# Performance work log

Hardware: AMD Instinct MI355X
Metric: run time of the kernel (lower is better)

## Reference

```python
import jax, jax.numpy as jnp
import numpy as np

DROPOUT_P = 0.1  # module-level constant in the source
DROP_KEY = jax.random.key(42)

B, H, S, D = 4, 16, 1024, 64


def setup_inputs() -> dict:
    key = jax.random.key(0)
    kq, kk, kv = jax.random.split(key, 3)
    return {
        "query": jax.random.normal(kq, (B, H, S, D), dtype=jnp.float32),
        "key": jax.random.normal(kk, (B, H, S, D), dtype=jnp.float32),
        "value": jax.random.normal(kv, (B, H, S, D), dtype=jnp.float32),
        "scale_factor": 8,
    }


def reference(query, key, value, scale_factor):
    # qk = query @ key^T                         [B,H,S,S]
    qk = jnp.einsum("bhqd,bhkd->bhqk", query, key)
    # source divides by inv_scale = 1/scale_factor -> multiply by scale_factor
    scaled_qk = qk * jnp.float32(scale_factor)
    softmax_qk = jax.nn.softmax(scaled_qk, axis=-1)
    # inverted dropout with fixed key (deterministic reference)
    keep = jax.random.bernoulli(DROP_KEY, 1.0 - DROPOUT_P, softmax_qk.shape)
    dropout_qk = jnp.where(keep, softmax_qk / (1.0 - DROPOUT_P), 0.0)
    # output = attn @ value                      [B,H,S,D]
    return jnp.einsum("bhqk,bhkd->bhqd", dropout_qk, value)
```

## Files before the change

### kernel.cpp

```cpp
#include <hip/hip_runtime.h>
#include <stdint.h>
#include <math.h>


constexpr int Bn = 4, Hn = 16, Sn = 1024, Dn = 64;
constexpr int NT = 256;
constexpr int TQ = 128, TK = 64;
constexpr int CAP = 256;

typedef short s16x8 __attribute__((ext_vector_type(8)));
typedef short s16x4 __attribute__((ext_vector_type(4)));
typedef float f32x4 __attribute__((ext_vector_type(4)));

__device__ __forceinline__ uint16_t f2bf(float x) {
  uint32_t u = __float_as_uint(x);
  return (uint16_t)((u + 0x7fffu + ((u >> 16) & 1u)) >> 16);
}
__device__ __forceinline__ float bf2f(uint16_t h) {
  return __uint_as_float(((uint32_t)h) << 16);
}

__device__ __forceinline__ void tf_round(uint32_t& x0, uint32_t& x1, const int r) {
  x0 += x1;
  x1 = (x1 << r) | (x1 >> (32 - r));
  x1 ^= x0;
}

__device__ __noinline__ int keep_bit(uint32_t j) {
  uint32_t x0 = 0u, x1 = j;
  const uint32_t k0 = 0u, k1v = 42u;
  const uint32_t k2v = k0 ^ k1v ^ 0x1BD11BDAu;
  x0 += k0; x1 += k1v;
  tf_round(x0, x1, 13); tf_round(x0, x1, 15); tf_round(x0, x1, 26); tf_round(x0, x1, 6);
  x0 += k1v; x1 += k2v + 1u;
  tf_round(x0, x1, 17); tf_round(x0, x1, 29); tf_round(x0, x1, 16); tf_round(x0, x1, 24);
  x0 += k2v; x1 += k0 + 2u;
  tf_round(x0, x1, 13); tf_round(x0, x1, 15); tf_round(x0, x1, 26); tf_round(x0, x1, 6);
  x0 += k0; x1 += k1v + 3u;
  tf_round(x0, x1, 17); tf_round(x0, x1, 29); tf_round(x0, x1, 16); tf_round(x0, x1, 24);
  x0 += k1v; x1 += k2v + 4u;
  tf_round(x0, x1, 13); tf_round(x0, x1, 15); tf_round(x0, x1, 26); tf_round(x0, x1, 6);
  x0 += k2v; x1 += k0 + 5u;
  uint32_t bits = x0 ^ x1;
  float u = __uint_as_float((bits >> 9) | 0x3f800000u) - 1.0f;
  return u < 0.9f;
}

__global__ __launch_bounds__(NT) void prep_kv(const float* __restrict__ K,
                                              const float* __restrict__ V,
                                              uint16_t* __restrict__ Khg,
                                              uint16_t* __restrict__ Klg,
                                              uint16_t* __restrict__ Vtg) {
  __shared__ float Vl[TK][Dn + 1];
  const int t = threadIdx.x;
  const int kt = blockIdx.x;
  const int bh = blockIdx.y;
  const int r = t >> 2, qd = t & 3;
  const size_t tile = ((size_t)bh * 16 + kt) * 4096;
  const float* ksrc = K + ((size_t)bh * Sn + (size_t)(kt * TK + r)) * Dn + qd * 16;
  const float* vsrc = V + ((size_t)bh * Sn + (size_t)(kt * TK + r)) * Dn + qd * 16;

#pragma unroll
  for (int half = 0; half < 2; ++half) {
    float4 a = *(const float4*)(ksrc + half * 8);
    float4 b = *(const float4*)(ksrc + half * 8 + 4);
    float xs[8] = {a.x, a.y, a.z, a.w, b.x, b.y, b.z, b.w};
    s16x8 hv, lv;
#pragma unroll
    for (int j = 0; j < 8; ++j) {
      uint16_t hb = f2bf(xs[j]);
      hv[j] = (short)hb;
      lv[j] = (short)f2bf(xs[j] - bf2f(hb));
    }
    const int sc = (qd * 2 + half) ^ (r & 7);
    *(s16x8*)&Khg[tile + (size_t)r * 64 + sc * 8] = hv;
    *(s16x8*)&Klg[tile + (size_t)r * 64 + sc * 8] = lv;
    float4 va = *(const float4*)(vsrc + half * 8);
    float4 vb = *(const float4*)(vsrc + half * 8 + 4);
    *(float4*)&Vl[r][qd * 16 + half * 8] = va;
    *(float4*)&Vl[r][qd * 16 + half * 8 + 4] = vb;
  }
  __syncthreads();
#pragma unroll
  for (int half = 0; half < 2; ++half) {
    s16x8 ov;
#pragma unroll
    for (int j = 0; j < 8; ++j) ov[j] = (short)f2bf(Vl[qd * 16 + half * 8 + j][r]);
    const int sc = (qd * 2 + half) ^ (r & 7);
    *(s16x8*)&Vtg[tile + (size_t)r * 64 + sc * 8] = ov;
  }
}

__global__ __launch_bounds__(NT, 2) void attn_mfma6(
    const float* __restrict__ Q, const uint16_t* __restrict__ Khg,
    const uint16_t* __restrict__ Klg, const uint16_t* __restrict__ Vtg,
    const float* __restrict__ V, const int* __restrict__ scale_ptr,
    float* __restrict__ out) {
  __shared__ uint16_t KhS[TK * Dn];
  __shared__ uint16_t KlS[TK * Dn];
  __shared__ uint16_t VtS[TK * Dn];
  __shared__ uint16_t PS[4 * 32 * 64];
  __shared__ uint32_t Lm[4][CAP];
  __shared__ float Lsv[4][CAP];
  __shared__ float mfin[4][32];

  const int t = threadIdx.x;
  const int w = t >> 6;
  const int lane = t & 63;
  const int l16 = lane & 15;
  const int quad = lane >> 4;
  const int xl = l16 & 7;

  const int b = blockIdx.z, h = blockIdx.y;
  const int qbase = blockIdx.x * TQ;
  const int bh = b * Hn + h;
  const float qscale = (float)(*scale_ptr);
  const float pthr = 1.670170079e-5f;

  const int e0off = (w * 2) * 512 + lane * 8;
  const int e1off = (w * 2 + 1) * 512 + lane * 8;
  const size_t tbase = (size_t)bh * 16 * 4096;
  const int psw = w * 2048;

  s16x8 qh[2][2], ql[2][2];
#pragma unroll
  for (int u = 0; u < 2; ++u) {
    const int qrow = qbase + w * 32 + u * 16 + l16;
    const float* src = Q + ((size_t)bh * Sn + (size_t)qrow) * Dn;
#pragma unroll
    for (int ks = 0; ks < 2; ++ks) {
      float4 x0 = *(const float4*)(src + ks * 32 + quad * 8);
      float4 x1 = *(const float4*)(src + ks * 32 + quad * 8 + 4);
      float xv[8] = {x0.x, x0.y, x0.z, x0.w, x1.x, x1.y, x1.z, x1.w};
#pragma unroll
      for (int j = 0; j < 8; ++j) {
        const float xs = xv[j] * qscale;
        uint16_t hb = f2bf(xs);
        qh[u][ks][j] = (short)hb;
        ql[u][ks][j] = (short)f2bf(xs - bf2f(hb));
      }
    }
  }

  float m_r[2] = {-INFINITY, -INFINITY};
  float l_r[2] = {0.0f, 0.0f};
  f32x4 o_acc[2][4];
#pragma unroll
  for (int u = 0; u < 2; ++u)
#pragma unroll
    for (int c = 0; c < 4; ++c) o_acc[u][c] = (f32x4){0.f, 0.f, 0.f, 0.f};

  const uint32_t hbase = (uint32_t)bh * (uint32_t)Sn;
  int lbase = 0;

  for (int kt = 0; kt < Sn / TK; ++kt) {
    const int kbase = kt * TK;
    __syncthreads();

    {
      const size_t tile = tbase + (size_t)kt * 4096;
      __builtin_amdgcn_global_load_lds(
          (const __attribute__((address_space(1))) uint32_t*)(Khg + tile + e0off),
          (__attribute__((address_space(3))) uint32_t*)(KhS + e0off), 16, 0, 0);
      __builtin_amdgcn_global_load_lds(
          (const __attribute__((address_space(1))) uint32_t*)(Khg + tile + e1off),
          (__attribute__((address_space(3))) uint32_t*)(KhS + e1off), 16, 0, 0);
      __builtin_amdgcn_global_load_lds(
          (const __attribute__((address_space(1))) uint32_t*)(Klg + tile + e0off),
          (__attribute__((address_space(3))) uint32_t*)(KlS + e0off), 16, 0, 0);
      __builtin_amdgcn_global_load_lds(
          (const __attribute__((address_space(1))) uint32_t*)(Klg + tile + e1off),
          (__attribute__((address_space(3))) uint32_t*)(KlS + e1off), 16, 0, 0);
      __builtin_amdgcn_global_load_lds(
          (const __attribute__((address_space(1))) uint32_t*)(Vtg + tile + e0off),
          (__attribute__((address_space(3))) uint32_t*)(VtS + e0off), 16, 0, 0);
      __builtin_amdgcn_global_load_lds(
          (const __attribute__((address_space(1))) uint32_t*)(Vtg + tile + e1off),
          (__attribute__((address_space(3))) uint32_t*)(VtS + e1off), 16, 0, 0);
    }
    __syncthreads();

    f32x4 sacc[2][4];
#pragma unroll
    for (int u = 0; u < 2; ++u)
#pragma unroll
      for (int c = 0; c < 4; ++c) sacc[u][c] = (f32x4){0.f, 0.f, 0.f, 0.f};
#pragma unroll
    for (int ks = 0; ks < 2; ++ks) {
#pragma unroll
      for (int c = 0; c < 4; ++c) {
        const int boff = (c * 16 + l16) * 64 + (((ks * 4 + quad) ^ xl) * 8);
        const s16x8 khv = *(const s16x8*)&KhS[boff];
        const s16x8 klv = *(const s16x8*)&KlS[boff];
#pragma unroll
        for (int u = 0; u < 2; ++u) {
          sacc[u][c] = __builtin_amdgcn_mfma_f32_16x16x32_bf16(khv, qh[u][ks], sacc[u][c], 0, 0, 0);
          sacc[u][c] = __builtin_amdgcn_mfma_f32_16x16x32_bf16(khv, ql[u][ks], sacc[u][c], 0, 0, 0);
          sacc[u][c] = __builtin_amdgcn_mfma_f32_16x16x32_bf16(klv, qh[u][ks], sacc[u][c], 0, 0, 0);
        }
      }
    }

#pragma unroll
    for (int u = 0; u < 2; ++u) {
      float mx = sacc[u][0][0];
#pragma unroll
      for (int c = 0; c < 4; ++c)
#pragma unroll
        for (int r = 0; r < 4; ++r) mx = fmaxf(mx, sacc[u][c][r]);
      mx = fmaxf(mx, __shfl_xor(mx, 16));
      mx = fmaxf(mx, __shfl_xor(mx, 32));
      const float mn = fmaxf(m_r[u], mx);
      const float al = __expf(m_r[u] - mn);
      m_r[u] = mn;
#pragma unroll
      for (int c = 0; c < 4; ++c)
#pragma unroll
        for (int r = 0; r < 4; ++r) o_acc[u][c][r] *= al;

      const bool anyhot = __ballot(mx - mn > -11.0f) != 0ull;
      float rs = 0.0f;
#pragma unroll
      for (int c = 0; c < 4; ++c) {
        float pc[4];
#pragma unroll
        for (int r = 0; r < 4; ++r) {
          pc[r] = __expf(sacc[u][c][r] - mn);
          rs += pc[r];
        }
        if (anyhot) {
#pragma unroll
          for (int r = 0; r < 4; ++r) {
            const uint64_t mc = __ballot(pc[r] > pthr);
            if (mc != 0ull) {
              if (lbase + 64 <= CAP) {
                const int slot = lbase + (int)__popcll(mc & ((1ull << lane) - 1ull));
                if (pc[r] > pthr) {
                  const uint32_t rw = (uint32_t)(u * 16 + l16);
                  Lm[w][slot] = (rw << 10) | (uint32_t)(kbase + c * 16 + quad * 4 + r);
                  Lsv[w][slot] = sacc[u][c][r];
                }
                lbase += (int)__popcll(mc);
              } else if (pc[r] > pthr) {
                const uint32_t j =
                    (hbase + (uint32_t)(qbase + w * 32 + u * 16 + l16)) * (uint32_t)Sn +
                    (uint32_t)(kbase + c * 16 + quad * 4 + r);
                if (!keep_bit(j)) pc[r] = 0.0f;
              }
            }
          }
        }
        s16x4 pk;
#pragma unroll
        for (int r = 0; r < 4; ++r) pk[r] = (short)f2bf(pc[r]);
        const int pos = (c * 2 + (quad >> 1)) ^ xl;
        *(s16x4*)&PS[psw + (u * 16 + l16) * 64 + pos * 8 + (quad & 1) * 4] = pk;
      }

      rs += __shfl_xor(rs, 16);
      rs += __shfl_xor(rs, 32);
      l_r[u] = l_r[u] * al + rs;
    }

#pragma unroll
    for (int ks2 = 0; ks2 < 2; ++ks2) {
      s16x8 pb[2];
#pragma unroll
      for (int u = 0; u < 2; ++u)
        pb[u] = *(const s16x8*)&PS[psw + (u * 16 + l16) * 64 + (((ks2 * 4 + quad) ^ xl) * 8)];
#pragma unroll
      for (int c = 0; c < 4; ++c) {
        const int voff = (c * 16 + l16) * 64 + (((ks2 * 4 + quad) ^ xl) * 8);
        const s16x8 vb = *(const s16x8*)&VtS[voff];
#pragma unroll
        for (int u = 0; u < 2; ++u)
          o_acc[u][c] = __builtin_amdgcn_mfma_f32_16x16x32_bf16(vb, pb[u], o_acc[u][c], 0, 0, 0);
      }
    }
  }

  if (quad == 0) {
#pragma unroll
    for (int u = 0; u < 2; ++u) mfin[w][u * 16 + l16] = m_r[u];
  }
  for (int e0 = 0; e0 < lbase; e0 += 64) {
    const int e = e0 + lane;
    const bool valid = e < lbase;
    const uint32_t meta = valid ? Lm[w][e] : 0u;
    const float sv = valid ? Lsv[w][e] : 0.0f;
    const uint32_t rwv = meta >> 10, keyv = meta & 1023u;
    const uint32_t grow = (uint32_t)(qbase + w * 32) + rwv;
    const uint32_t j = (hbase + grow) * (uint32_t)Sn + keyv;
    const int kb = keep_bit(j);
    uint64_t dm = __ballot(valid && !kb);
    while (dm != 0ull) {
      const int src = (int)__builtin_ctzll(dm);
      dm &= dm - 1ull;
      const uint32_t meta_s = (uint32_t)__builtin_amdgcn_readlane((int)meta, src);
      const float sv_s =
          __uint_as_float((uint32_t)__builtin_amdgcn_readlane((int)__float_as_uint(sv), src));
      const int rw = (int)(meta_s >> 10);
      const int key = (int)(meta_s & 1023u);
      const float p = __expf(sv_s - mfin[w][rw]);
      const float pb2 = bf2f(f2bf(p));
      if ((rw & 15) == l16) {
        const float* vp = V + ((size_t)bh * Sn + (size_t)key) * Dn;
        if ((rw >> 4) == 0) {
#pragma unroll
          for (int c = 0; c < 4; ++c) {
            float4 vv = *(const float4*)(vp + c * 16 + quad * 4);
            o_acc[0][c][0] = fmaf(-pb2, bf2f(f2bf(vv.x)), o_acc[0][c][0]);
            o_acc[0][c][1] = fmaf(-pb2, bf2f(f2bf(vv.y)), o_acc[0][c][1]);
            o_acc[0][c][2] = fmaf(-pb2, bf2f(f2bf(vv.z)), o_acc[0][c][2]);
            o_acc[0][c][3] = fmaf(-pb2, bf2f(f2bf(vv.w)), o_acc[0][c][3]);
          }
        } else {
#pragma unroll
          for (int c = 0; c < 4; ++c) {
            float4 vv = *(const float4*)(vp + c * 16 + quad * 4);
            o_acc[1][c][0] = fmaf(-pb2, bf2f(f2bf(vv.x)), o_acc[1][c][0]);
            o_acc[1][c][1] = fmaf(-pb2, bf2f(f2bf(vv.y)), o_acc[1][c][1]);
            o_acc[1][c][2] = fmaf(-pb2, bf2f(f2bf(vv.z)), o_acc[1][c][2]);
            o_acc[1][c][3] = fmaf(-pb2, bf2f(f2bf(vv.w)), o_acc[1][c][3]);
          }
        }
      }
    }
  }

#pragma unroll
  for (int u = 0; u < 2; ++u) {
    const float inv = 1.0f / (l_r[u] * 0.9f);
    const size_t obase = ((size_t)bh * Sn + (size_t)(qbase + w * 32 + u * 16 + l16)) * Dn;
#pragma unroll
    for (int c = 0; c < 4; ++c) {
      float4 ov;
      ov.x = o_acc[u][c][0] * inv;
      ov.y = o_acc[u][c][1] * inv;
      ov.z = o_acc[u][c][2] * inv;
      ov.w = o_acc[u][c][3] * inv;
      *(float4*)(out + obase + c * 16 + quad * 4) = ov;
    }
  }
}

constexpr int KST = 72;
__global__ __launch_bounds__(NT) void attn_fallback(
    const float* __restrict__ Q, const float* __restrict__ K,
    const float* __restrict__ V, const int* __restrict__ scale_ptr,
    float* __restrict__ out) {
  __shared__ uint16_t KhS[64 * KST];
  __shared__ uint16_t KlS[64 * KST];
  __shared__ uint16_t VtS[Dn * KST];
  __shared__ uint16_t PSf[4 * 16 * KST];

  const int t = threadIdx.x;
  const int w = t >> 6;
  const int lane = t & 63;
  const int l16 = lane & 15;
  const int quad = lane >> 4;
  const int b = blockIdx.z, h = blockIdx.y;
  const int qbase = blockIdx.x * 64;
  const size_t bh = (size_t)b * Hn + h;
  const float scale = (float)(*scale_ptr);
  const float* Kp = K + bh * Sn * Dn;
  const float* Vp = V + bh * Sn * Dn;

  const int qrow = qbase + w * 16 + l16;
  const float* Qp = Q + (bh * Sn + (size_t)qrow) * Dn;
  s16x8 qh[2], ql[2];
#pragma unroll
  for (int ks = 0; ks < 2; ++ks) {
    const float* src = Qp + ks * 32 + quad * 8;
    float4 x0 = *(const float4*)(src);
    float4 x1 = *(const float4*)(src + 4);
    float xv[8] = {x0.x, x0.y, x0.z, x0.w, x1.x, x1.y, x1.z, x1.w};
#pragma unroll
    for (int j = 0; j < 8; ++j) {
      uint16_t hb = f2bf(xv[j]);
      qh[ks][j] = (short)hb;
      ql[ks][j] = (short)f2bf(xv[j] - bf2f(hb));
    }
  }
  const int kr = t >> 2;
  const int qd = t & 3;
  float m_r[4], l_r[4];
#pragma unroll
  for (int r = 0; r < 4; ++r) { m_r[r] = -INFINITY; l_r[r] = 0.0f; }
  f32x4 o_acc[4];
#pragma unroll
  for (int c = 0; c < 4; ++c) o_acc[c] = (f32x4){0.f, 0.f, 0.f, 0.f};
  const uint32_t rowlin = ((uint32_t)(b * Hn + h)) * (uint32_t)Sn +
                          (uint32_t)(qbase + w * 16 + quad * 4);
  for (int kt = 0; kt < Sn / 64; ++kt) {
    const int kbase = kt * 64;
    __syncthreads();
    {
      const float* ksrc = Kp + (size_t)(kbase + kr) * Dn + qd * 16;
#pragma unroll
      for (int half = 0; half < 2; ++half) {
        float4 a = *(const float4*)(ksrc + half * 8);
        float4 b2 = *(const float4*)(ksrc + half * 8 + 4);
        float xs[8] = {a.x, a.y, a.z, a.w, b2.x, b2.y, b2.z, b2.w};
        s16x8 hv, lv;
#pragma unroll
        for (int j = 0; j < 8; ++j) {
          uint16_t hb = f2bf(xs[j]);
          hv[j] = (short)hb;
          lv[j] = (short)f2bf(xs[j] - bf2f(hb));
        }
        *(s16x8*)&KhS[kr * KST + qd * 16 + half * 8] = hv;
        *(s16x8*)&KlS[kr * KST + qd * 16 + half * 8] = lv;
      }
      const float* vsrc = Vp + (size_t)(kbase + kr) * Dn + qd * 16;
#pragma unroll
      for (int half = 0; half < 2; ++half) {
        float4 a = *(const float4*)(vsrc + half * 8);
        float4 b2 = *(const float4*)(vsrc + half * 8 + 4);
        float xs[8] = {a.x, a.y, a.z, a.w, b2.x, b2.y, b2.z, b2.w};
#pragma unroll
        for (int j = 0; j < 8; ++j)
          VtS[(qd * 16 + half * 8 + j) * KST + kr] = f2bf(xs[j]);
      }
    }
    __syncthreads();
    f32x4 sacc[4];
#pragma unroll
    for (int c = 0; c < 4; ++c) sacc[c] = (f32x4){0.f, 0.f, 0.f, 0.f};
#pragma unroll
    for (int ks = 0; ks < 2; ++ks) {
#pragma unroll
      for (int c = 0; c < 4; ++c) {
        const s16x8 bh_ = *(const s16x8*)&KhS[(c * 16 + l16) * KST + ks * 32 + quad * 8];
        const s16x8 bl_ = *(const s16x8*)&KlS[(c * 16 + l16) * KST + ks * 32 + quad * 8];
        sacc[c] = __builtin_amdgcn_mfma_f32_16x16x32_bf16(qh[ks], bh_, sacc[c], 0, 0, 0);
        sacc[c] = __builtin_amdgcn_mfma_f32_16x16x32_bf16(ql[ks], bh_, sacc[c], 0, 0, 0);
        sacc[c] = __builtin_amdgcn_mfma_f32_16x16x32_bf16(qh[ks], bl_, sacc[c], 0, 0, 0);
      }
    }
    float mx[4];
#pragma unroll
    for (int r = 0; r < 4; ++r) {
      mx[r] = sacc[0][r] * scale;
#pragma unroll
      for (int c = 1; c < 4; ++c) mx[r] = fmaxf(mx[r], sacc[c][r] * scale);
#pragma unroll
      for (int d = 1; d < 16; d <<= 1) mx[r] = fmaxf(mx[r], __shfl_xor(mx[r], d));
    }
    float al[4];
#pragma unroll
    for (int r = 0; r < 4; ++r) {
      const float mn = fmaxf(m_r[r], mx[r]);
      al[r] = __expf(m_r[r] - mn);
      m_r[r] = mn;
    }
#pragma unroll
    for (int c = 0; c < 4; ++c)
#pragma unroll
      for (int r = 0; r < 4; ++r) o_acc[c][r] *= al[r];
    float rs[4] = {0.f, 0.f, 0.f, 0.f};
#pragma unroll
    for (int c = 0; c < 4; ++c) {
#pragma unroll
      for (int r = 0; r < 4; ++r) {
        const float d = sacc[c][r] * scale - m_r[r];
        float pv = __expf(d);
        rs[r] += pv;
        if (d > -25.0f) {
          const uint32_t j = (rowlin + (uint32_t)r) * (uint32_t)Sn +
                             (uint32_t)(kbase + c * 16 + l16);
          if (!keep_bit(j)) pv = 0.0f;
        }
        PSf[(w * 16 + quad * 4 + r) * KST + c * 16 + l16] = f2bf(pv);
      }
    }
#pragma unroll
    for (int r = 0; r < 4; ++r) {
#pragma unroll
      for (int d = 1; d < 16; d <<= 1) rs[r] += __shfl_xor(rs[r], d);
      l_r[r] = l_r[r] * al[r] + rs[r];
    }
#pragma unroll
    for (int ks2 = 0; ks2 < 2; ++ks2) {
      const s16x8 pa = *(const s16x8*)&PSf[(w * 16 + l16) * KST + ks2 * 32 + quad * 8];
#pragma unroll
      for (int c = 0; c < 4; ++c) {
        const s16x8 vb = *(const s16x8*)&VtS[(c * 16 + l16) * KST + ks2 * 32 + quad * 8];
        o_acc[c] = __builtin_amdgcn_mfma_f32_16x16x32_bf16(pa, vb, o_acc[c], 0, 0, 0);
      }
    }
  }
  float inv[4];
#pragma unroll
  for (int r = 0; r < 4; ++r) inv[r] = 1.0f / (l_r[r] * 0.9f);
#pragma unroll
  for (int c = 0; c < 4; ++c)
#pragma unroll
    for (int r = 0; r < 4; ++r)
      out[(bh * Sn + (size_t)(qbase + w * 16 + quad * 4 + r)) * Dn + c * 16 + l16] =
          o_acc[c][r] * inv[r];
}

extern "C" void kernel_launch(void* const* d_in, const int* in_sizes, int n_in,
                              void* d_out, int out_size, void* d_ws, size_t ws_size,
                              hipStream_t stream) {
  const float* Q = (const float*)d_in[0];
  const float* K = (const float*)d_in[1];
  const float* V = (const float*)d_in[2];
  const int* sf = (const int*)d_in[3];
  float* out = (float*)d_out;

  constexpr size_t ARR = (size_t)Bn * Hn * Sn * Dn;
  const size_t need = 3 * ARR * sizeof(uint16_t);

  if (ws_size >= need) {
    uint16_t* Khg = (uint16_t*)d_ws;
    uint16_t* Klg = Khg + ARR;
    uint16_t* Vtg = Klg + ARR;
    prep_kv<<<dim3(16, 64), NT, 0, stream>>>(K, V, Khg, Klg, Vtg);
    attn_mfma6<<<dim3(Sn / TQ, Hn, Bn), NT, 0, stream>>>(Q, Khg, Klg, Vtg, V, sf, out);
  } else {
    attn_fallback<<<dim3(Sn / 64, Hn, Bn), NT, 0, stream>>>(Q, K, V, sf, out);
  }
}
```

Before: 185.4 us.

## Halve query tile per block to 64 rows and raise occupancy to four blocks

Each wave now handles 16 query rows instead of 32, so the per-block query tile shrinks from 128 to 64 and the grid doubles. Register and LDS use per block drop (one accumulator set, smaller P buffer and sparse-list capacity), which allows launch bounds of 4 blocks per CU. In exchange, each K/V tile is loaded from global and staged in LDS twice as often per query row, since fewer rows share it. The smaller sparse-entry list may also overflow into the slower in-loop dropout path more often.

```diff
diff --git a/kernel.cpp b/kernel.cpp
--- a/kernel.cpp
+++ b/kernel.cpp
@@ -5,8 +5,9 @@
 
 constexpr int Bn = 4, Hn = 16, Sn = 1024, Dn = 64;
 constexpr int NT = 256;
-constexpr int TQ = 128, TK = 64;
-constexpr int CAP = 256;
+constexpr int TK = 64;
+constexpr int TQM = 64;
+constexpr int CAP = 128;
 
 typedef short s16x8 __attribute__((ext_vector_type(8)));
 typedef short s16x4 __attribute__((ext_vector_type(4)));
@@ -91,7 +92,7 @@
   }
 }
 
-__global__ __launch_bounds__(NT, 2) void attn_mfma6(
+__global__ __launch_bounds__(NT, 4) void attn_mfma7(
     const float* __restrict__ Q, const uint16_t* __restrict__ Khg,
     const uint16_t* __restrict__ Klg, const uint16_t* __restrict__ Vtg,
     const float* __restrict__ V, const int* __restrict__ scale_ptr,
@@ -99,10 +100,10 @@
   __shared__ uint16_t KhS[TK * Dn];
   __shared__ uint16_t KlS[TK * Dn];
   __shared__ uint16_t VtS[TK * Dn];
-  __shared__ uint16_t PS[4 * 32 * 64];
+  __shared__ uint16_t PS[4 * 16 * 64];
   __shared__ uint32_t Lm[4][CAP];
   __shared__ float Lsv[4][CAP];
-  __shared__ float mfin[4][32];
+  __shared__ float mfin[4][16];
 
   const int t = threadIdx.x;
   const int w = t >> 6;
@@ -112,7 +113,7 @@
   const int xl = l16 & 7;
 
   const int b = blockIdx.z, h = blockIdx.y;
-  const int qbase = blockIdx.x * TQ;
+  const int qbase = blockIdx.x * TQM;
   const int bh = b * Hn + h;
   const float qscale = (float)(*scale_ptr);
   const float pthr = 1.670170079e-5f;
@@ -120,12 +121,11 @@
   const int e0off = (w * 2) * 512 + lane * 8;
   const int e1off = (w * 2 + 1) * 512 + lane * 8;
   const size_t tbase = (size_t)bh * 16 * 4096;
-  const int psw = w * 2048;
-
-  s16x8 qh[2][2], ql[2][2];
-#pragma unroll
-  for (int u = 0; u < 2; ++u) {
-    const int qrow = qbase + w * 32 + u * 16 + l16;
+  const int psw = w * 1024;
+
+  s16x8 qh[2], ql[2];
+  {
+    const int qrow = qbase + w * 16 + l16;
     const float* src = Q + ((size_t)bh * Sn + (size_t)qrow) * Dn;
 #pragma unroll
     for (int ks = 0; ks < 2; ++ks) {
@@ -136,19 +136,16 @@
       for (int j = 0; j < 8; ++j) {
         const float xs = xv[j] * qscale;
         uint16_t hb = f2bf(xs);
-        qh[u][ks][j] = (short)hb;
-        ql[u][ks][j] = (short)f2bf(xs - bf2f(hb));
-      }
-    }
-  }
-
-  float m_r[2] = {-INFINITY, -INFINITY};
-  float l_r[2] = {0.0f, 0.0f};
-  f32x4 o_acc[2][4];
-#pragma unroll
-  for (int u = 0; u < 2; ++u)
-#pragma unroll
-    for (int c = 0; c < 4; ++c) o_acc[u][c] = (f32x4){0.f, 0.f, 0.f, 0.f};
+        qh[ks][j] = (short)hb;
+        ql[ks][j] = (short)f2bf(xs - bf2f(hb));
+      }
+    }
+  }
+
+  float m_r = -INFINITY, l_r = 0.0f;
+  f32x4 o_acc[4];
+#pragma unroll
+  for (int c = 0; c < 4; ++c) o_acc[c] = (f32x4){0.f, 0.f, 0.f, 0.f};
 
   const uint32_t hbase = (uint32_t)bh * (uint32_t)Sn;
   int lbase = 0;
@@ -180,11 +177,9 @@
     }
     __syncthreads();
 
-    f32x4 sacc[2][4];
-#pragma unroll
-    for (int u = 0; u < 2; ++u)
-#pragma unroll
-      for (int c = 0; c < 4; ++c) sacc[u][c] = (f32x4){0.f, 0.f, 0.f, 0.f};
+    f32x4 sacc[4];
+#pragma unroll
+    for (int c = 0; c < 4; ++c) sacc[c] = (f32x4){0.f, 0.f, 0.f, 0.f};
 #pragma unroll
     for (int ks = 0; ks < 2; ++ks) {
 #pragma unroll
@@ -192,31 +187,27 @@
         const int boff = (c * 16 + l16) * 64 + (((ks * 4 + quad) ^ xl) * 8);
         const s16x8 khv = *(const s16x8*)&KhS[boff];
         const s16x8 klv = *(const s16x8*)&KlS[boff];
-#pragma unroll
-        for (int u = 0; u < 2; ++u) {
-          sacc[u][c] = __builtin_amdgcn_mfma_f32_16x16x32_bf16(khv, qh[u][ks], sacc[u][c], 0, 0, 0);
-          sacc[u][c] = __builtin_amdgcn_mfma_f32_16x16x32_bf16(khv, ql[u][ks], sacc[u][c], 0, 0, 0);
-          sacc[u][c] = __builtin_amdgcn_mfma_f32_16x16x32_bf16(klv, qh[u][ks], sacc[u][c], 0, 0, 0);
-        }
-      }
-    }
-
-#pragma unroll
-    for (int u = 0; u < 2; ++u) {
-      float mx = sacc[u][0][0];
+        sacc[c] = __builtin_amdgcn_mfma_f32_16x16x32_bf16(khv, qh[ks], sacc[c], 0, 0, 0);
+        sacc[c] = __builtin_amdgcn_mfma_f32_16x16x32_bf16(khv, ql[ks], sacc[c], 0, 0, 0);
+        sacc[c] = __builtin_amdgcn_mfma_f32_16x16x32_bf16(klv, qh[ks], sacc[c], 0, 0, 0);
+      }
+    }
+
+    {
+      float mx = sacc[0][0];
 #pragma unroll
       for (int c = 0; c < 4; ++c)
 #pragma unroll
-        for (int r = 0; r < 4; ++r) mx = fmaxf(mx, sacc[u][c][r]);
+        for (int r = 0; r < 4; ++r) mx = fmaxf(mx, sacc[c][r]);
       mx = fmaxf(mx, __shfl_xor(mx, 16));
       mx = fmaxf(mx, __shfl_xor(mx, 32));
-      const float mn = fmaxf(m_r[u], mx);
-      const float al = __expf(m_r[u] - mn);
-      m_r[u] = mn;
+      const float mn = fmaxf(m_r, mx);
+      const float al = __expf(m_r - mn);
+      m_r = mn;
 #pragma unroll
       for (int c = 0; c < 4; ++c)
 #pragma unroll
-        for (int r = 0; r < 4; ++r) o_acc[u][c][r] *= al;
+        for (int r = 0; r < 4; ++r) o_acc[c][r] *= al;
 
       const bool anyhot = __ballot(mx - mn > -11.0f) != 0ull;
       float rs = 0.0f;
@@ -225,7 +216,7 @@
         float pc[4];
 #pragma unroll
         for (int r = 0; r < 4; ++r) {
-          pc[r] = __expf(sacc[u][c][r] - mn);
+          pc[r] = __expf(sacc[c][r] - mn);
           rs += pc[r];
         }
         if (anyhot) {
@@ -236,14 +227,14 @@
               if (lbase + 64 <= CAP) {
                 const int slot = lbase + (int)__popcll(mc & ((1ull << lane) - 1ull));
                 if (pc[r] > pthr) {
-                  const uint32_t rw = (uint32_t)(u * 16 + l16);
-                  Lm[w][slot] = (rw << 10) | (uint32_t)(kbase + c * 16 + quad * 4 + r);
-                  Lsv[w][slot] = sacc[u][c][r];
+                  Lm[w][slot] = ((uint32_t)l16 << 10) |
+                                (uint32_t)(kbase + c * 16 + quad * 4 + r);
+                  Lsv[w][slot] = sacc[c][r];
                 }
                 lbase += (int)__popcll(mc);
               } else if (pc[r] > pthr) {
                 const uint32_t j =
-                    (hbase + (uint32_t)(qbase + w * 32 + u * 16 + l16)) * (uint32_t)Sn +
+                    (hbase + (uint32_t)(qbase + w * 16 + l16)) * (uint32_t)Sn +
                     (uint32_t)(kbase + c * 16 + quad * 4 + r);
                 if (!keep_bit(j)) pc[r] = 0.0f;
               }
@@ -254,42 +245,34 @@
 #pragma unroll
         for (int r = 0; r < 4; ++r) pk[r] = (short)f2bf(pc[r]);
         const int pos = (c * 2 + (quad >> 1)) ^ xl;
-        *(s16x4*)&PS[psw + (u * 16 + l16) * 64 + pos * 8 + (quad & 1) * 4] = pk;
+        *(s16x4*)&PS[psw + l16 * 64 + pos * 8 + (quad & 1) * 4] = pk;
       }
 
       rs += __shfl_xor(rs, 16);
       rs += __shfl_xor(rs, 32);
-      l_r[u] = l_r[u] * al + rs;
+      l_r = l_r * al + rs;
     }
 
 #pragma unroll
     for (int ks2 = 0; ks2 < 2; ++ks2) {
-      s16x8 pb[2];
-#pragma unroll
-      for (int u = 0; u < 2; ++u)
-        pb[u] = *(const s16x8*)&PS[psw + (u * 16 + l16) * 64 + (((ks2 * 4 + quad) ^ xl) * 8)];
+      const s16x8 pb = *(const s16x8*)&PS[psw + l16 * 64 + (((ks2 * 4 + quad) ^ xl) * 8)];
 #pragma unroll
       for (int c = 0; c < 4; ++c) {
         const int voff = (c * 16 + l16) * 64 + (((ks2 * 4 + quad) ^ xl) * 8);
         const s16x8 vb = *(const s16x8*)&VtS[voff];
-#pragma unroll
-        for (int u = 0; u < 2; ++u)
-          o_acc[u][c] = __builtin_amdgcn_mfma_f32_16x16x32_bf16(vb, pb[u], o_acc[u][c], 0, 0, 0);
-      }
-    }
-  }
-
-  if (quad == 0) {
-#pragma unroll
-    for (int u = 0; u < 2; ++u) mfin[w][u * 16 + l16] = m_r[u];
-  }
+        o_acc[c] = __builtin_amdgcn_mfma_f32_16x16x32_bf16(vb, pb, o_acc[c], 0, 0, 0);
+      }
+    }
+  }
+
+  if (quad == 0) mfin[w][l16] = m_r;
   for (int e0 = 0; e0 < lbase; e0 += 64) {
     const int e = e0 + lane;
     const bool valid = e < lbase;
     const uint32_t meta = valid ? Lm[w][e] : 0u;
     const float sv = valid ? Lsv[w][e] : 0.0f;
     const uint32_t rwv = meta >> 10, keyv = meta & 1023u;
-    const uint32_t grow = (uint32_t)(qbase + w * 32) + rwv;
+    const uint32_t grow = (uint32_t)(qbase + w * 16) + rwv;
     const uint32_t j = (hbase + grow) * (uint32_t)Sn + keyv;
     const int kb = keep_bit(j);
     uint64_t dm = __ballot(valid && !kb);
@@ -303,42 +286,30 @@
       const int key = (int)(meta_s & 1023u);
       const float p = __expf(sv_s - mfin[w][rw]);
       const float pb2 = bf2f(f2bf(p));
-      if ((rw & 15) == l16) {
+      if (rw == l16) {
         const float* vp = V + ((size_t)bh * Sn + (size_t)key) * Dn;
-        if ((rw >> 4) == 0) {
-#pragma unroll
-          for (int c = 0; c < 4; ++c) {
-            float4 vv = *(const float4*)(vp + c * 16 + quad * 4);
-            o_acc[0][c][0] = fmaf(-pb2, bf2f(f2bf(vv.x)), o_acc[0][c][0]);
-            o_acc[0][c][1] = fmaf(-pb2, bf2f(f2bf(vv.y)), o_acc[0][c][1]);
-            o_acc[0][c][2] = fmaf(-pb2, bf2f(f2bf(vv.z)), o_acc[0][c][2]);
-            o_acc[0][c][3] = fmaf(-pb2, bf2f(f2bf(vv.w)), o_acc[0][c][3]);
-          }
-        } else {
-#pragma unroll
-          for (int c = 0; c < 4; ++c) {
-            float4 vv = *(const float4*)(vp + c * 16 + quad * 4);
-            o_acc[1][c][0] = fmaf(-pb2, bf2f(f2bf(vv.x)), o_acc[1][c][0]);
-            o_acc[1][c][1] = fmaf(-pb2, bf2f(f2bf(vv.y)), o_acc[1][c][1]);
-            o_acc[1][c][2] = fmaf(-pb2, bf2f(f2bf(vv.z)), o_acc[1][c][2]);
-            o_acc[1][c][3] = fmaf(-pb2, bf2f(f2bf(vv.w)), o_acc[1][c][3]);
-          }
+#pragma unroll
+        for (int c = 0; c < 4; ++c) {
+          float4 vv = *(const float4*)(vp + c * 16 + quad * 4);
+          o_acc[c][0] = fmaf(-pb2, bf2f(f2bf(vv.x)), o_acc[c][0]);
+          o_acc[c][1] = fmaf(-pb2, bf2f(f2bf(vv.y)), o_acc[c][1]);
+          o_acc[c][2] = fmaf(-pb2, bf2f(f2bf(vv.z)), o_acc[c][2]);
+          o_acc[c][3] = fmaf(-pb2, bf2f(f2bf(vv.w)), o_acc[c][3]);
         }
       }
     }
   }
 
-#pragma unroll
-  for (int u = 0; u < 2; ++u) {
-    const float inv = 1.0f / (l_r[u] * 0.9f);
-    const size_t obase = ((size_t)bh * Sn + (size_t)(qbase + w * 32 + u * 16 + l16)) * Dn;
+  {
+    const float inv = 1.0f / (l_r * 0.9f);
+    const size_t obase = ((size_t)bh * Sn + (size_t)(qbase + w * 16 + l16)) * Dn;
 #pragma unroll
     for (int c = 0; c < 4; ++c) {
       float4 ov;
-      ov.x = o_acc[u][c][0] * inv;
-      ov.y = o_acc[u][c][1] * inv;
-      ov.z = o_acc[u][c][2] * inv;
-      ov.w = o_acc[u][c][3] * inv;
+      ov.x = o_acc[c][0] * inv;
+      ov.y = o_acc[c][1] * inv;
+      ov.z = o_acc[c][2] * inv;
+      ov.w = o_acc[c][3] * inv;
       *(float4*)(out + obase + c * 16 + quad * 4) = ov;
     }
   }
@@ -518,7 +489,7 @@
     uint16_t* Klg = Khg + ARR;
     uint16_t* Vtg = Klg + ARR;
     prep_kv<<<dim3(16, 64), NT, 0, stream>>>(K, V, Khg, Klg, Vtg);
-    attn_mfma6<<<dim3(Sn / TQ, Hn, Bn), NT, 0, stream>>>(Q, Khg, Klg, Vtg, V, sf, out);
+    attn_mfma7<<<dim3(Sn / TQM, Hn, Bn), NT, 0, stream>>>(Q, Khg, Klg, Vtg, V, sf, out);
   } else {
     attn_fallback<<<dim3(Sn / 64, Hn, Bn), NT, 0, stream>>>(Q, K, V, sf, out);
   }
```

Measured after the change: 169.5 us. 8.6% less time.
